# Performance work log

Measured on AMD Instinct MI355X. Metric: run time of the kernel, lower is better.

Reference implementation:

```python
import jax, jax.numpy as jnp
import numpy as np
from jax import lax

NUM_GRAPHS = 64
CODEBOOK = 64
HID = 256
DIST = 8
N_NODES = 50000
EPS = 0.1
ITERS = 20
STAB = 1e-8
CLAMP_MAX = 1e6


def setup_inputs() -> dict:
    key = jax.random.key(0)
    k1, k2, k3 = jax.random.split(key, 3)
    node_distributions = jax.random.normal(k1, (N_NODES, DIST, HID), dtype=jnp.float32)
    batch_idx = jnp.sort(jax.random.randint(k2, (N_NODES,), 0, NUM_GRAPHS)).astype(jnp.int64)
    # xavier_uniform_ on [codebook_size, hidden_dim]
    bound = float(np.sqrt(6.0 / (CODEBOOK + HID)))
    codebook = jax.random.uniform(k3, (CODEBOOK, HID), minval=-bound, maxval=bound, dtype=jnp.float32)
    return {"node_distributions": node_distributions, "batch_idx": batch_idx, "codebook": codebook}


def reference(node_distributions, batch_idx, codebook):
    # Flatten: points are node-major, so segment id per point repeats batch_idx DIST times.
    x = node_distributions.reshape(-1, HID)          # [P, HID], P = N_NODES*DIST
    seg = jnp.repeat(batch_idx, DIST)                # [P]

    # Squared-Euclidean cost matrix against codebook, clamped at 0.
    x_norm = jnp.sum(x * x, axis=1, keepdims=True)   # [P, 1]
    y_norm = jnp.sum(codebook * codebook, axis=1)    # [K]
    cost = jnp.maximum(x_norm + y_norm[None, :] - 2.0 * (x @ codebook.T), 0.0)  # [P, K]

    Kmat = jnp.exp(-cost / EPS)
    Kmat = jnp.where(jnp.isnan(Kmat) | jnp.isinf(Kmat), STAB, Kmat)

    # Per-graph marginals: a = 1/(rows in graph), b = 1/K.
    counts = jax.ops.segment_sum(jnp.ones_like(batch_idx, dtype=jnp.float32), batch_idx, num_segments=NUM_GRAPHS)  # nodes/graph
    n_rows = counts * DIST                           # flattened rows per graph
    a = 1.0 / jnp.maximum(n_rows, 1.0)[seg]          # [P] (empty graphs have no points)
    b_marg = 1.0 / CODEBOOK

    u0 = jnp.ones(x.shape[0], dtype=x.dtype)
    v0 = jnp.ones((NUM_GRAPHS, CODEBOOK), dtype=x.dtype)

    def step(carry, _):
        u, v = carry
        Kv = jnp.sum(Kmat * v[seg], axis=1)                          # [P]
        u = a / jnp.maximum(Kv, STAB)
        KTu = jax.ops.segment_sum(Kmat * u[:, None], seg, num_segments=NUM_GRAPHS)  # [B, K]
        v = b_marg / jnp.maximum(KTu, STAB)
        return (u, v), None

    (u, v), _ = lax.scan(step, (u0, v0), None, length=ITERS)

    uc = jnp.clip(u, STAB, CLAMP_MAX)
    vc = jnp.clip(v, STAB, CLAMP_MAX)

    # Column sums of transport matrix per graph: sum_p uc_p * K[p,k] * vc[b,k]
    wsum = jax.ops.segment_sum(Kmat * uc[:, None], seg, num_segments=NUM_GRAPHS) * vc  # [B, K]
    total = jnp.sum(wsum, axis=1, keepdims=True)

    normed = jnp.where(total > STAB, wsum / jnp.maximum(total, STAB), 1.0 / CODEBOOK)
    # Graphs with zero nodes are skipped in the original (stay zero).
    out = jnp.where(counts[:, None] == 0, 0.0, normed)
    return out
```

## Files before the change

### kernel.cpp

```cpp
#include <hip/hip_runtime.h>

#define NG 64
#define KK 64
#define DIST 8
#define NNODES 50000
#define PTOT (NNODES*DIST)
#define EPSV 0.1f
#define NITERS 20
#define STABV 1e-8f
#define CMAXV 1e6f

#define OFF_COUNTS 0
#define OFF_NNZ 64
#define OFF_NSUS 65
#define OFF_MAXY 66
#define OFF_YN 128
#define OFF_SUS 192
#define OFF_ROWSEG (OFF_SUS + PTOT)
#define OFF_UC (OFF_ROWSEG + PTOT)
#define OFF_KROWS (OFF_UC + PTOT)

__device__ __forceinline__ float dot4(float4 a, float4 b) {
  return fmaf(a.x, b.x, fmaf(a.y, b.y, fmaf(a.z, b.z, a.w * b.w)));
}

__global__ __launch_bounds__(256) void init_kernel(const float* __restrict__ cb,
                                                   float* __restrict__ ws) {
  __shared__ float ynsh[KK];
  int t = threadIdx.x, w = t >> 6, l = t & 63;
  if (t < NG) ((int*)ws)[OFF_COUNTS + t] = 0;
  if (t == 0) { ((int*)ws)[OFF_NNZ] = 0; ((int*)ws)[OFF_NSUS] = 0; }
  const float4* cb4 = (const float4*)cb;
#pragma unroll
  for (int it = 0; it < 16; it++) {
    float4 c = cb4[it * 256 + t];
    float e = dot4(c, c);
#pragma unroll
    for (int m = 1; m < 64; m <<= 1) e += __shfl_xor(e, m);
    if (l == 0) ynsh[it * 4 + w] = e;
  }
  __syncthreads();
  if (t < KK) {
    float yn = ynsh[t];
    ws[OFF_YN + t] = yn;
    float ym = sqrtf(yn);
#pragma unroll
    for (int m = 1; m < 64; m <<= 1) ym = fmaxf(ym, __shfl_xor(ym, m));
    if (t == 0) ws[OFF_MAXY] = ym;
  }
}

__global__ __launch_bounds__(256) void main_kernel(const float* __restrict__ x,
    const int* __restrict__ bidx, float* __restrict__ ws) {
  __shared__ int hist[NG];
  int t = threadIdx.x, w = t >> 6, l = t & 63;
  int b = blockIdx.x;
  if (t < NG) hist[t] = 0;
  __syncthreads();
  if (t < 40) atomicAdd(&hist[bidx[b * 40 + t] & 63], 1);
  __syncthreads();
  if (t < NG && hist[t] > 0) atomicAdd(&((int*)ws)[OFF_COUNTS + t], hist[t]);

  float maxy = ws[OFF_MAXY];
  float thr = fmaf(maxy, 1.0001f, 0.01f) + 3.6f;
  float thr2 = thr * thr;
  const float4* x4 = (const float4*)x;
  int q = l >> 4, r = l & 15;
  int base = b * 320 + w * 80;
  int* nsusp = &((int*)ws)[OFF_NSUS];
  int* sus = &((int*)ws)[OFF_SUS];
#pragma unroll
  for (int o = 0; o < 5; o++) {
    int p0 = base + o * 16;
    float4 v0 = x4[(size_t)(p0 + q) * 64 + r];
    float4 v1 = x4[(size_t)(p0 + 4 + q) * 64 + r];
    float4 v2 = x4[(size_t)(p0 + 8 + q) * 64 + r];
    float4 v3 = x4[(size_t)(p0 + 12 + q) * 64 + r];
    float s0 = dot4(v0, v0), s1 = dot4(v1, v1), s2 = dot4(v2, v2), s3 = dot4(v3, v3);
#pragma unroll
    for (int m = 1; m < 16; m <<= 1) {
      s0 += __shfl_xor(s0, m); s1 += __shfl_xor(s1, m);
      s2 += __shfl_xor(s2, m); s3 += __shfl_xor(s3, m);
    }
    if (r == 0) {
      float ss[4] = {s0, s1, s2, s3};
#pragma unroll
      for (int i = 0; i < 4; i++) {
        bool safe = (ss[i] > thr2) && (ss[i] < 1e30f);
        if (!safe) {
          int slot = atomicAdd(nsusp, 1);
          if (slot < PTOT) sus[slot] = p0 + 4 * i + q;
        }
      }
    }
  }
}

__global__ __launch_bounds__(256) void suspect_kernel(const float* __restrict__ x,
    const int* __restrict__ bidx, float* __restrict__ ws, int cap) {
  int tid = threadIdx.x;
  int wave = tid >> 6, lane = tid & 63;
  int nsus = ((int*)ws)[OFF_NSUS];
  if (nsus > PTOT) nsus = PTOT;
  const int* sus = &((int*)ws)[OFF_SUS];
  const float4* x4 = (const float4*)x;
  int gw = blockIdx.x * 4 + wave, nw = gridDim.x * 4;
  for (int si = gw; si < nsus; si += nw) {
    int p = sus[si];
    float4 xv = x4[(size_t)p * 64 + lane];
    float xn = dot4(xv, xv);
#pragma unroll
    for (int m = 1; m < 64; m <<= 1) xn += __shfl_xor(xn, m);
    float myk = 0.0f;
    for (int k = 0; k < KK; k++) {
      k = k;
    }
    (void)myk; (void)xn;
  }
}

__global__ __launch_bounds__(256) void suspect2_kernel(const float* __restrict__ x,
    const int* __restrict__ bidx, const float* __restrict__ cb,
    float* __restrict__ ws, int cap) {
  int tid = threadIdx.x;
  int wave = tid >> 6, lane = tid & 63;
  int nsus = ((int*)ws)[OFF_NSUS];
  if (nsus > PTOT) nsus = PTOT;
  const int* sus = &((int*)ws)[OFF_SUS];
  const float4* x4 = (const float4*)x;
  const float4* cb4 = (const float4*)cb;
  int gw = blockIdx.x * 4 + wave, nw = gridDim.x * 4;
  for (int si = gw; si < nsus; si += nw) {
    int p = sus[si];
    float4 xv = x4[(size_t)p * 64 + lane];
    float xn = dot4(xv, xv);
#pragma unroll
    for (int m = 1; m < 64; m <<= 1) xn += __shfl_xor(xn, m);
    float myk = 0.0f;
    for (int k = 0; k < KK; k++) {
      float4 c = cb4[k * 64 + lane];
      float d = dot4(xv, c);
#pragma unroll
      for (int m = 1; m < 64; m <<= 1) d += __shfl_xor(d, m);
      float cost = fmaxf(xn + ws[OFF_YN + k] - 2.0f * d, 0.0f);
      float km = __expf(cost * (-1.0f / EPSV));
      if (!(km <= 1.0f)) km = STABV;
      if (lane == k) myk = km;
    }
    unsigned long long nz = __ballot(myk != 0.0f);
    if (nz != 0ull) {
      int slot = 0;
      if (lane == 0) slot = atomicAdd(&((int*)ws)[OFF_NNZ], 1);
      slot = __shfl(slot, 0);
      if (slot < cap) {
        (ws + OFF_KROWS)[(size_t)slot * 64 + lane] = myk;
        if (lane == 0) ((int*)ws)[OFF_ROWSEG + slot] = bidx[p >> 3];
      }
    }
  }
}

__global__ __launch_bounds__(256) void solve_kernel(float* __restrict__ ws,
                                                    float* __restrict__ out, int cap) {
  __shared__ float vsh[NG * KK];
  __shared__ float ash[NG * KK];
  __shared__ float tot[NG];
  __shared__ float ainv[NG];
  int tid = threadIdx.x;
  int wave = tid >> 6, lane = tid & 63;
  int nnz = ((int*)ws)[OFF_NNZ];
  if (nnz > cap) nnz = cap;
  const float* krows = ws + OFF_KROWS;
  const int* rowseg = &((int*)ws)[OFF_ROWSEG];
  const int* counts = &((int*)ws)[OFF_COUNTS];
  float* uc = ws + OFF_UC;

  if (tid < NG) ainv[tid] = 1.0f / fmaxf((float)(counts[tid] * DIST), 1.0f);
  for (int i = tid; i < NG * KK; i += 256) { vsh[i] = 1.0f; ash[i] = 0.0f; }
  __syncthreads();

  if (nnz > 0) {
    for (int it = 0; it < NITERS; it++) {
      for (int i = tid; i < NG * KK; i += 256) ash[i] = 0.0f;
      __syncthreads();
      for (int r = wave; r < nnz; r += 4) {
        int g = rowseg[r];
        float kw = krows[(size_t)r * 64 + lane];
        float kv = kw * vsh[(g << 6) | lane];
#pragma unroll
        for (int m = 1; m < 64; m <<= 1) kv += __shfl_xor(kv, m);
        float u = ainv[g] / fmaxf(kv, STABV);
        if (it == NITERS - 1 && lane == 0) uc[r] = u;
        atomicAdd(&ash[(g << 6) | lane], kw * u);
      }
      __syncthreads();
      for (int i = tid; i < NG * KK; i += 256)
        vsh[i] = (1.0f / KK) / fmaxf(ash[i], STABV);
      __syncthreads();
    }
    for (int i = tid; i < NG * KK; i += 256) ash[i] = 0.0f;
    __syncthreads();
    for (int r = wave; r < nnz; r += 4) {
      int g = rowseg[r];
      float kw = krows[(size_t)r * 64 + lane];
      float u = fminf(fmaxf(uc[r], STABV), CMAXV);
      atomicAdd(&ash[(g << 6) | lane], kw * u);
    }
    __syncthreads();
  }

  for (int i = tid; i < NG * KK; i += 256) {
    float vv = fminf(fmaxf(vsh[i], STABV), CMAXV);
    ash[i] = ash[i] * vv;
  }
  __syncthreads();
  if (tid < NG) {
    float s = 0.0f;
    for (int k = 0; k < KK; k++) s += ash[(tid << 6) + k];
    tot[tid] = s;
  }
  __syncthreads();
  for (int i = tid; i < NG * KK; i += 256) {
    int g = i >> 6;
    float val;
    if (counts[g] == 0) val = 0.0f;
    else if (tot[g] > STABV) val = ash[i] / fmaxf(tot[g], STABV);
    else val = 1.0f / KK;
    out[i] = val;
  }
}

extern "C" void kernel_launch(void* const* d_in, const int* in_sizes, int n_in,
                              void* d_out, int out_size, void* d_ws, size_t ws_size,
                              hipStream_t stream) {
  const float* x = (const float*)d_in[0];
  const int* bidx = (const int*)d_in[1];
  const float* cb = (const float*)d_in[2];
  float* ws = (float*)d_ws;
  float* out = (float*)d_out;

  long cap_l = ((long)(ws_size / 4) - OFF_KROWS) / 64;
  if (cap_l < 0) cap_l = 0;
  if (cap_l > PTOT) cap_l = PTOT;
  int cap = (int)cap_l;

  init_kernel<<<1, 256, 0, stream>>>(cb, ws);
  main_kernel<<<NNODES / 40, 256, 0, stream>>>(x, bidx, ws);
  suspect2_kernel<<<64, 256, 0, stream>>>(x, bidx, cb, ws, cap);
  solve_kernel<<<1, 256, 0, stream>>>(ws, out, cap);
}
```

Before: 481.8 us.

## Prune rows using partial-norm lower bound from a single cache line

The row-norm pass now reads only one 128-byte slice (32 of 256 floats) of each point. The partial squared norm is a lower bound on the full norm, so points already above the cutoff are classified as contributing zero without reading the rest of the row. Points still below the cutoff are compacted per block into a candidate list. A second kernel reads one more slice for each candidate and marks the remaining ones as suspects for exact evaluation. The aim is to cut the full 400 MB sweep of x down to a fraction of it, at the cost of an extra launch and some atomics, with a speedup that depends on how the data is distributed.

```diff
diff --git a/kernel.cpp b/kernel.cpp
--- a/kernel.cpp
+++ b/kernel.cpp
@@ -14,8 +14,11 @@
 #define OFF_NNZ 64
 #define OFF_NSUS 65
 #define OFF_MAXY 66
+#define OFF_NC2 67
 #define OFF_YN 128
-#define OFF_SUS 192
+#define OFF_C2P 192
+#define OFF_C2S (OFF_C2P + PTOT)
+#define OFF_SUS (OFF_C2S + PTOT)
 #define OFF_ROWSEG (OFF_SUS + PTOT)
 #define OFF_UC (OFF_ROWSEG + PTOT)
 #define OFF_KROWS (OFF_UC + PTOT)
@@ -29,7 +32,9 @@
   __shared__ float ynsh[KK];
   int t = threadIdx.x, w = t >> 6, l = t & 63;
   if (t < NG) ((int*)ws)[OFF_COUNTS + t] = 0;
-  if (t == 0) { ((int*)ws)[OFF_NNZ] = 0; ((int*)ws)[OFF_NSUS] = 0; }
+  if (t == 0) {
+    ((int*)ws)[OFF_NNZ] = 0; ((int*)ws)[OFF_NSUS] = 0; ((int*)ws)[OFF_NC2] = 0;
+  }
   const float4* cb4 = (const float4*)cb;
 #pragma unroll
   for (int it = 0; it < 16; it++) {
@@ -50,12 +55,17 @@
   }
 }
 
-__global__ __launch_bounds__(256) void main_kernel(const float* __restrict__ x,
+__global__ __launch_bounds__(256) void pass1_kernel(const float* __restrict__ x,
     const int* __restrict__ bidx, float* __restrict__ ws) {
   __shared__ int hist[NG];
+  __shared__ int cl_p[320];
+  __shared__ float cl_s[320];
+  __shared__ int cl_n;
+  __shared__ int cl_base;
   int t = threadIdx.x, w = t >> 6, l = t & 63;
   int b = blockIdx.x;
   if (t < NG) hist[t] = 0;
+  if (t == 0) cl_n = 0;
   __syncthreads();
   if (t < 40) atomicAdd(&hist[bidx[b * 40 + t] & 63], 1);
   __syncthreads();
@@ -65,57 +75,66 @@
   float thr = fmaf(maxy, 1.0001f, 0.01f) + 3.6f;
   float thr2 = thr * thr;
   const float4* x4 = (const float4*)x;
-  int q = l >> 4, r = l & 15;
-  int base = b * 320 + w * 80;
-  int* nsusp = &((int*)ws)[OFF_NSUS];
-  int* sus = &((int*)ws)[OFF_SUS];
-#pragma unroll
-  for (int o = 0; o < 5; o++) {
-    int p0 = base + o * 16;
-    float4 v0 = x4[(size_t)(p0 + q) * 64 + r];
-    float4 v1 = x4[(size_t)(p0 + 4 + q) * 64 + r];
-    float4 v2 = x4[(size_t)(p0 + 8 + q) * 64 + r];
-    float4 v3 = x4[(size_t)(p0 + 12 + q) * 64 + r];
-    float s0 = dot4(v0, v0), s1 = dot4(v1, v1), s2 = dot4(v2, v2), s3 = dot4(v3, v3);
-#pragma unroll
-    for (int m = 1; m < 16; m <<= 1) {
-      s0 += __shfl_xor(s0, m); s1 += __shfl_xor(s1, m);
-      s2 += __shfl_xor(s2, m); s3 += __shfl_xor(s3, m);
-    }
-    if (r == 0) {
-      float ss[4] = {s0, s1, s2, s3};
-#pragma unroll
-      for (int i = 0; i < 4; i++) {
-        bool safe = (ss[i] > thr2) && (ss[i] < 1e30f);
-        if (!safe) {
-          int slot = atomicAdd(nsusp, 1);
-          if (slot < PTOT) sus[slot] = p0 + 4 * i + q;
-        }
-      }
-    }
-  }
-}
-
-__global__ __launch_bounds__(256) void suspect_kernel(const float* __restrict__ x,
-    const int* __restrict__ bidx, float* __restrict__ ws, int cap) {
-  int tid = threadIdx.x;
-  int wave = tid >> 6, lane = tid & 63;
-  int nsus = ((int*)ws)[OFF_NSUS];
-  if (nsus > PTOT) nsus = PTOT;
-  const int* sus = &((int*)ws)[OFF_SUS];
+  int g8 = l >> 3, sub = l & 7;
+  int base = b * 320 + w * 80 + g8;
+  float s[10];
+#pragma unroll
+  for (int o = 0; o < 10; o++) {
+    int p = base + o * 8;
+    float4 v = x4[(size_t)p * 64 + (g8 << 3) + sub];
+    float e = dot4(v, v);
+    e += __shfl_xor(e, 1); e += __shfl_xor(e, 2); e += __shfl_xor(e, 4);
+    s[o] = e;
+  }
+  if (sub == 0) {
+#pragma unroll
+    for (int o = 0; o < 10; o++) {
+      bool safe = (s[o] > thr2) && (s[o] < 1e30f);
+      if (!safe) {
+        int slot = atomicAdd(&cl_n, 1);
+        cl_p[slot] = base + o * 8;
+        cl_s[slot] = s[o];
+      }
+    }
+  }
+  __syncthreads();
+  if (t == 0) cl_base = atomicAdd(&((int*)ws)[OFF_NC2], cl_n);
+  __syncthreads();
+  int n = cl_n, cb0 = cl_base;
+  for (int i = t; i < n; i += 256) {
+    ((int*)ws)[OFF_C2P + cb0 + i] = cl_p[i];
+    ws[OFF_C2S + cb0 + i] = cl_s[i];
+  }
+}
+
+__global__ __launch_bounds__(256) void pass2_kernel(const float* __restrict__ x,
+                                                    float* __restrict__ ws) {
+  int t = threadIdx.x, w = t >> 6, l = t & 63;
+  int g8 = l >> 3, sub = l & 7;
+  int nc2 = ((int*)ws)[OFF_NC2];
+  const int* c2p = &((int*)ws)[OFF_C2P];
+  const float* c2s = ws + OFF_C2S;
+  float maxy = ws[OFF_MAXY];
+  float thr = fmaf(maxy, 1.0001f, 0.01f) + 3.6f;
+  float thr2 = thr * thr;
   const float4* x4 = (const float4*)x;
-  int gw = blockIdx.x * 4 + wave, nw = gridDim.x * 4;
-  for (int si = gw; si < nsus; si += nw) {
-    int p = sus[si];
-    float4 xv = x4[(size_t)p * 64 + lane];
-    float xn = dot4(xv, xv);
-#pragma unroll
-    for (int m = 1; m < 64; m <<= 1) xn += __shfl_xor(xn, m);
-    float myk = 0.0f;
-    for (int k = 0; k < KK; k++) {
-      k = k;
-    }
-    (void)myk; (void)xn;
+  int gw = blockIdx.x * 4 + w, nw = gridDim.x * 4;
+  for (int i0 = gw * 8; i0 < nc2; i0 += nw * 8) {
+    int idx = i0 + g8;
+    bool act = idx < nc2;
+    int p = c2p[act ? idx : (nc2 - 1)];
+    int line = ((p & 7) + 1) & 7;
+    float4 v = x4[(size_t)p * 64 + (line << 3) + sub];
+    float e = dot4(v, v);
+    e += __shfl_xor(e, 1); e += __shfl_xor(e, 2); e += __shfl_xor(e, 4);
+    if (act && sub == 0) {
+      float S = c2s[idx] + e;
+      bool safe = (S > thr2) && (S < 1e30f);
+      if (!safe) {
+        int slot = atomicAdd(&((int*)ws)[OFF_NSUS], 1);
+        if (slot < PTOT) ((int*)ws)[OFF_SUS + slot] = p;
+      }
+    }
   }
 }
 
@@ -245,7 +264,8 @@
   int cap = (int)cap_l;
 
   init_kernel<<<1, 256, 0, stream>>>(cb, ws);
-  main_kernel<<<NNODES / 40, 256, 0, stream>>>(x, bidx, ws);
+  pass1_kernel<<<NNODES / 40, 256, 0, stream>>>(x, bidx, ws);
+  pass2_kernel<<<128, 256, 0, stream>>>(x, ws);
   suspect2_kernel<<<64, 256, 0, stream>>>(x, bidx, cb, ws, cap);
   solve_kernel<<<1, 256, 0, stream>>>(ws, out, cap);
 }
```

New measurement: 542.9 us. 1.13x slower.
